# Performance work log

Measured on AMD Instinct MI355X. Metric: run time of the kernel, lower is better.

Reference implementation:

```python
import jax, jax.numpy as jnp
import numpy as np

N_NODES = 100000
N_EDGES = 1600000
NFEAT = 256
NHID = 64
NHEADS = 8
NCLASS = 97
ALPHA = 0.2  # leaky relu slope
EPS = 1e-16  # guard against isolated rows (pyGAT divides by e_rowsum directly)


def _sp_gat_layer(x, Wk, ak, src, dst, n_nodes, alpha, concat):
    """One SpGraphAttentionLayer (eval mode, dropout off).
    x: [N, f_in], Wk: [f_in, f_out], ak: [2*f_out].
    edge e_ij = exp(-leakyrelu(a . [h_i || h_j])), out[i] = sum_j e_ij h_j / sum_j e_ij.
    """
    h = x @ Wk                          # [N, f_out]
    f_out = Wk.shape[1]
    s_src = h @ ak[:f_out]              # [N] = a1 . h_i
    s_dst = h @ ak[f_out:]              # [N] = a2 . h_j
    e = jnp.exp(-jax.nn.leaky_relu(s_src[src] + s_dst[dst], negative_slope=alpha))  # [E]
    rowsum = jax.ops.segment_sum(e, src, num_segments=n_nodes)                       # [N]
    num = jax.ops.segment_sum(e[:, None] * h[dst], src, num_segments=n_nodes)        # [N, f_out]
    h_prime = num / (rowsum[:, None] + EPS)
    return jax.nn.elu(h_prime) if concat else h_prime


def setup_inputs() -> dict:
    key = jax.random.key(0)
    ks = jax.random.split(key, 6)
    gain = 1.414  # xavier gain used by pyGAT
    features = jax.random.normal(ks[0], (N_NODES, NFEAT), dtype=jnp.float32)
    edge_index = jax.random.randint(ks[1], (2, N_EDGES), 0, N_NODES, dtype=jnp.int64)
    W = jax.random.normal(ks[2], (NHEADS, NFEAT, NHID), dtype=jnp.float32) * (gain * np.sqrt(2.0 / (NFEAT + NHID)))
    a = jax.random.normal(ks[3], (NHEADS, 2 * NHID), dtype=jnp.float32) * (gain * np.sqrt(2.0 / (1 + 2 * NHID)))
    W_out = jax.random.normal(ks[4], (NHEADS * NHID, NCLASS), dtype=jnp.float32) * (gain * np.sqrt(2.0 / (NHEADS * NHID + NCLASS)))
    a_out = jax.random.normal(ks[5], (2 * NCLASS,), dtype=jnp.float32) * (gain * np.sqrt(2.0 / (1 + 2 * NCLASS)))
    return {"features": features, "W": W, "a": a, "W_out": W_out, "a_out": a_out, "edge_index": edge_index}


def reference(features, W, a, W_out, a_out, edge_index):
    src, dst = edge_index[0], edge_index[1]
    n = features.shape[0]
    # multi-head hidden layer, concat heads (loop over small fixed head count to bound memory)
    heads = [
        _sp_gat_layer(features, W[k], a[k], src, dst, n, ALPHA, concat=True)
        for k in range(W.shape[0])
    ]
    x = jnp.concatenate(heads, axis=1)  # [N, nheads*nhid]
    # output attention layer (concat=False), then elu + log_softmax as in SpGAT.forward
    x = _sp_gat_layer(x, W_out, a_out, src, dst, n, ALPHA, concat=False)
    return jax.nn.log_softmax(jax.nn.elu(x), axis=1)
```

## Files before the change

### kernel.cpp

```cpp
#include <hip/hip_runtime.h>
#include <hip/hip_bf16.h>
#include <stdint.h>

typedef __attribute__((ext_vector_type(8))) short short8;
typedef __attribute__((ext_vector_type(4))) float floatx4;
typedef uint32_t u32;

#define N_NODES 100000
#define N_EDGES 1600000
#define ALPHA_SLOPE 0.2f
#define EPS_F 1e-16f

static __device__ __forceinline__ float bf2f(ushort h) {
    u32 u = ((u32)h) << 16;
    return __builtin_bit_cast(float, u);
}
static __device__ __forceinline__ ushort f2bf(float f) {
    u32 u = __builtin_bit_cast(u32, f);
    u32 r = (u + 0x7fffu + ((u >> 16) & 1u)) >> 16;
    return (ushort)r;
}
static __device__ __forceinline__ float edge_e(float s) {
    float lr = s > 0.f ? s : ALPHA_SLOPE * s;
    return __expf(-lr);
}

__global__ __launch_bounds__(256) void prep(
    const float* __restrict__ feat, const float* __restrict__ W,
    const float* __restrict__ Wout, const float* __restrict__ a,
    const float* __restrict__ aout, const int* __restrict__ ei,
    ushort* __restrict__ featb, ushort* __restrict__ Bp1, ushort* __restrict__ Bp2,
    float* __restrict__ acol1, float* __restrict__ acol2, int* __restrict__ cnt)
{
    int b = blockIdx.x;
    if (b < 25000) {
        int i = b * 256 + threadIdx.x;
        float4 v = ((const float4*)feat)[i];
        ushort4 o;
        o.x = f2bf(v.x); o.y = f2bf(v.y); o.z = f2bf(v.z); o.w = f2bf(v.w);
        ((ushort4*)featb)[i] = o;
    } else if (b < 25512) {
        int idx = (b - 25000) * 256 + threadIdx.x;
        if (idx < 256 * 512) {
            int k = idx >> 9, n = idx & 511;
            int head = n >> 6, c = n & 63;
            Bp1[((size_t)(k >> 3) * 512 + n) * 8 + (k & 7)] = f2bf(W[head * 16384 + k * 64 + c]);
        }
        if (idx < 512 * 128) {
            int k = idx >> 7, n = idx & 127;
            ushort v = (n < 97) ? f2bf(Wout[k * 97 + n]) : (ushort)0;
            Bp2[((size_t)(k >> 3) * 128 + n) * 8 + (k & 7)] = v;
        }
        if (idx < 512) {
            int head = idx >> 6, c = idx & 63;
            acol1[idx * 2]     = a[head * 128 + c];
            acol1[idx * 2 + 1] = a[head * 128 + 64 + c];
        }
        if (idx < 128) {
            acol2[idx * 2]     = (idx < 97) ? aout[idx] : 0.f;
            acol2[idx * 2 + 1] = (idx < 97) ? aout[97 + idx] : 0.f;
        }
    } else {
        int e = (b - 25512) * 256 + threadIdx.x;
        atomicAdd(&cnt[ei[e]], 1);
    }
}

__global__ __launch_bounds__(256) void gemm_mfma(
    const ushort* __restrict__ A, const ushort* __restrict__ Bp,
    ushort* __restrict__ C, const float* __restrict__ acol,
    float* __restrict__ ssrc_arr, float* __restrict__ sdst_arr,
    int sstride, int M, int K, int NP)
{
    __shared__ __align__(16) ushort Ald[8 * 128 * 8];
    const int tid = threadIdx.x;
    const int lane = tid & 63;
    const int wave = tid >> 6;
    const int wr = wave >> 1, wc = wave & 1;
    const int row0 = blockIdx.y * 128;
    const int col0 = blockIdx.x * 128;
    const int quad = lane >> 4;
    const int l16 = lane & 15;

    floatx4 acc[4][4] = {};

    for (int k0 = 0; k0 < K; k0 += 64) {
        __syncthreads();
#pragma unroll
        for (int i = 0; i < 4; ++i) {
            int q = i * 256 + tid;
            int r = q >> 3, kq = q & 7;
            int row = row0 + r;
            if (row >= M) row = M - 1;
            const uint4* src = (const uint4*)(A + (size_t)row * K + k0 + kq * 8);
            *(uint4*)(&Ald[(kq * 128 + (r ^ kq)) * 8]) = *src;
        }
        __syncthreads();

#pragma unroll
        for (int s = 0; s < 2; ++s) {
            int kqq = s * 4 + quad;
            int kqg = (k0 >> 3) + kqq;
            short8 bfrag[4];
#pragma unroll
            for (int nt = 0; nt < 4; ++nt) {
                int col = col0 + wc * 64 + nt * 16 + l16;
                bfrag[nt] = *(const short8*)(Bp + ((size_t)kqg * NP + col) * 8);
            }
#pragma unroll
            for (int mt = 0; mt < 4; ++mt) {
                int r = wr * 64 + mt * 16 + l16;
                short8 afrag = *(const short8*)(&Ald[(kqq * 128 + (r ^ kqq)) * 8]);
#pragma unroll
                for (int nt = 0; nt < 4; ++nt) {
                    acc[mt][nt] = __builtin_amdgcn_mfma_f32_16x16x32_bf16(afrag, bfrag[nt], acc[mt][nt], 0, 0, 0);
                }
            }
        }
    }

#pragma unroll
    for (int mt = 0; mt < 4; ++mt) {
#pragma unroll
        for (int rr = 0; rr < 4; ++rr) {
            int row = row0 + wr * 64 + mt * 16 + quad * 4 + rr;
            if (row < M) {
#pragma unroll
                for (int nt = 0; nt < 4; ++nt) {
                    int col = col0 + wc * 64 + nt * 16 + l16;
                    C[(size_t)row * NP + col] = f2bf(acc[mt][nt][rr]);
                }
            }
        }
    }

    float av1[4], av2[4];
#pragma unroll
    for (int nt = 0; nt < 4; ++nt) {
        int col = col0 + wc * 64 + nt * 16 + l16;
        av1[nt] = acol[col * 2];
        av2[nt] = acol[col * 2 + 1];
    }
    int g = (col0 + wc * 64) >> 6;
    int goff = (sstride > 1) ? g : 0;
#pragma unroll
    for (int mt = 0; mt < 4; ++mt) {
#pragma unroll
        for (int rr = 0; rr < 4; ++rr) {
            float p1 = 0.f, p2 = 0.f;
#pragma unroll
            for (int nt = 0; nt < 4; ++nt) {
                p1 = fmaf(acc[mt][nt][rr], av1[nt], p1);
                p2 = fmaf(acc[mt][nt][rr], av2[nt], p2);
            }
#pragma unroll
            for (int o = 1; o < 16; o <<= 1) {
                p1 += __shfl_xor(p1, o);
                p2 += __shfl_xor(p2, o);
            }
            int row = row0 + wr * 64 + mt * 16 + quad * 4 + rr;
            if (l16 == 0 && row < M) {
                atomicAdd(&ssrc_arr[(size_t)row * sstride + goff], p1);
                atomicAdd(&sdst_arr[(size_t)row * sstride + goff], p2);
            }
        }
    }
}

__global__ __launch_bounds__(256) void scan_partial(const int* __restrict__ cnt, int* __restrict__ bsum, int N) {
    int idx = blockIdx.x * 256 + threadIdx.x;
    int v = (idx < N) ? cnt[idx] : 0;
#pragma unroll
    for (int o = 32; o; o >>= 1) v += __shfl_xor(v, o);
    __shared__ int ws[4];
    if ((threadIdx.x & 63) == 0) ws[threadIdx.x >> 6] = v;
    __syncthreads();
    if (threadIdx.x == 0) bsum[blockIdx.x] = ws[0] + ws[1] + ws[2] + ws[3];
}

__global__ __launch_bounds__(512) void scan_block(int* __restrict__ bsum, int nb) {
    __shared__ int s[512];
    int t = threadIdx.x;
    int v = (t < nb) ? bsum[t] : 0;
    s[t] = v;
    __syncthreads();
    for (int o = 1; o < 512; o <<= 1) {
        int u = (t >= o) ? s[t - o] : 0;
        __syncthreads();
        s[t] += u;
        __syncthreads();
    }
    if (t < nb) bsum[t] = s[t] - v;
}

__global__ __launch_bounds__(256) void scan_final(
    const int* __restrict__ cnt, const int* __restrict__ bsum,
    int* __restrict__ row_ptr, int N, int E)
{
    int b = blockIdx.x, t = threadIdx.x;
    int idx = b * 256 + t;
    int v = (idx < N) ? cnt[idx] : 0;
    __shared__ int s[256];
    s[t] = v;
    __syncthreads();
    for (int o = 1; o < 256; o <<= 1) {
        int u = (t >= o) ? s[t - o] : 0;
        __syncthreads();
        s[t] += u;
        __syncthreads();
    }
    if (idx < N) row_ptr[idx] = bsum[b] + s[t] - v;
    if (idx == 0) row_ptr[N] = E;
}

__global__ __launch_bounds__(256) void fill_csr(
    const int* __restrict__ ei, const int* __restrict__ row_ptr,
    int* __restrict__ cur, int* __restrict__ col_idx, int E)
{
    int e = blockIdx.x * 256 + threadIdx.x;
    if (e >= E) return;
    int s = ei[e];
    int d = ei[E + e];
    int p = atomicAdd(&cur[s], 1);
    col_idx[row_ptr[s] + p] = d;
}

__global__ __launch_bounds__(256, 6) void ea1p(
    const int* __restrict__ row_ptr, const int* __restrict__ col_idx,
    const ushort* __restrict__ h_all, const float* __restrict__ ssrc1,
    const float* __restrict__ sdst1, const ushort* __restrict__ Bp2,
    const float* __restrict__ acol2, ushort* __restrict__ h2p,
    float* __restrict__ s2src, float* __restrict__ s2dst)
{
    __shared__ __align__(16) ushort Xs[16 * 512];
    const int tid = threadIdx.x;
    const int l = tid & 63;
    const int wv = tid >> 6;
    const int hl = l >> 3;
    const int blk = blockIdx.x;

#pragma unroll 1
    for (int i = 0; i < 4; ++i) {
        int r = wv * 4 + i;
        int node = __builtin_amdgcn_readfirstlane(blk * 16 + r);
        int start = row_ptr[node], end = row_ptr[node + 1];
        float si = ssrc1[(size_t)node * 8 + hl];
        float acc[8] = {};
        float re = 0.f;
        int j = start;
        for (; j + 4 <= end; j += 4) {
            int d0 = col_idx[j], d1 = col_idx[j + 1], d2 = col_idx[j + 2], d3 = col_idx[j + 3];
            float e0 = edge_e(si + sdst1[(size_t)d0 * 8 + hl]);
            float e1 = edge_e(si + sdst1[(size_t)d1 * 8 + hl]);
            float e2 = edge_e(si + sdst1[(size_t)d2 * 8 + hl]);
            float e3 = edge_e(si + sdst1[(size_t)d3 * 8 + hl]);
            short8 v0 = *(const short8*)(h_all + (size_t)d0 * 512 + l * 8);
            short8 v1 = *(const short8*)(h_all + (size_t)d1 * 512 + l * 8);
            short8 v2 = *(const short8*)(h_all + (size_t)d2 * 512 + l * 8);
            short8 v3 = *(const short8*)(h_all + (size_t)d3 * 512 + l * 8);
            re += (e0 + e1) + (e2 + e3);
#pragma unroll
            for (int q = 0; q < 8; ++q) {
                float t0 = fmaf(e0, bf2f((ushort)v0[q]), e1 * bf2f((ushort)v1[q]));
                float t1 = fmaf(e2, bf2f((ushort)v2[q]), e3 * bf2f((ushort)v3[q]));
                acc[q] += t0 + t1;
            }
        }
        for (; j < end; ++j) {
            int d = col_idx[j];
            float e = edge_e(si + sdst1[(size_t)d * 8 + hl]);
            short8 hv = *(const short8*)(h_all + (size_t)d * 512 + l * 8);
            re += e;
#pragma unroll
            for (int q = 0; q < 8; ++q)
                acc[q] = fmaf(e, bf2f((ushort)hv[q]), acc[q]);
        }
        float inv = 1.f / (re + EPS_F);
        short8 o;
#pragma unroll
        for (int q = 0; q < 8; ++q) {
            float p = acc[q] * inv;
            p = p > 0.f ? p : expm1f(p);
            o[q] = (short)f2bf(p);
        }
        *(short8*)(&Xs[((size_t)r * 64 + (size_t)(l ^ (r & 7))) * 8]) = o;
    }
    __syncthreads();

    const int l16 = l & 15;
    const int g = l >> 4;
    floatx4 acc2[2] = {};
#pragma unroll
    for (int s = 0; s < 16; ++s) {
        int c = s * 4 + g;
        short8 afrag = *(const short8*)(&Xs[((size_t)l16 * 64 + (size_t)(c ^ (l16 & 7))) * 8]);
#pragma unroll
        for (int nt = 0; nt < 2; ++nt) {
            int col = wv * 32 + nt * 16 + l16;
            short8 bfrag = *(const short8*)(Bp2 + ((size_t)c * 128 + col) * 8);
            acc2[nt] = __builtin_amdgcn_mfma_f32_16x16x32_bf16(afrag, bfrag, acc2[nt], 0, 0, 0);
        }
    }

    float av1[2], av2[2];
#pragma unroll
    for (int nt = 0; nt < 2; ++nt) {
        int col = wv * 32 + nt * 16 + l16;
        av1[nt] = acol2[col * 2];
        av2[nt] = acol2[col * 2 + 1];
    }
#pragma unroll
    for (int rr = 0; rr < 4; ++rr) {
        int row = g * 4 + rr;
        int node = blk * 16 + row;
        float p1 = 0.f, p2 = 0.f;
#pragma unroll
        for (int nt = 0; nt < 2; ++nt) {
            int col = wv * 32 + nt * 16 + l16;
            h2p[(size_t)node * 128 + col] = f2bf(acc2[nt][rr]);
            p1 = fmaf(acc2[nt][rr], av1[nt], p1);
            p2 = fmaf(acc2[nt][rr], av2[nt], p2);
        }
#pragma unroll
        for (int o = 1; o < 16; o <<= 1) {
            p1 += __shfl_xor(p1, o);
            p2 += __shfl_xor(p2, o);
        }
        if (l16 == 0) {
            atomicAdd(&s2src[node], p1);
            atomicAdd(&s2dst[node], p2);
        }
    }
}

__global__ __launch_bounds__(256) void ea2(
    const int* __restrict__ row_ptr, const int* __restrict__ col_idx,
    const ushort* __restrict__ h2p, const float* __restrict__ s2src,
    const float* __restrict__ s2dst, float* __restrict__ out)
{
    int w = blockIdx.x * 8 + (threadIdx.x >> 5);
    int l = threadIdx.x & 31;
    int start = row_ptr[w], end = row_ptr[w + 1];
    float si = s2src[w];
    float a0 = 0.f, a1 = 0.f, a2 = 0.f, a3 = 0.f, re = 0.f;
    int j = start;
    for (; j + 4 <= end; j += 4) {
        int d0 = col_idx[j], d1 = col_idx[j + 1], d2 = col_idx[j + 2], d3 = col_idx[j + 3];
        float e0 = edge_e(si + s2dst[d0]);
        float e1 = edge_e(si + s2dst[d1]);
        float e2 = edge_e(si + s2dst[d2]);
        float e3 = edge_e(si + s2dst[d3]);
        ushort4 h0 = *(const ushort4*)(h2p + (size_t)d0 * 128 + 4 * l);
        ushort4 h1 = *(const ushort4*)(h2p + (size_t)d1 * 128 + 4 * l);
        ushort4 h2 = *(const ushort4*)(h2p + (size_t)d2 * 128 + 4 * l);
        ushort4 h3 = *(const ushort4*)(h2p + (size_t)d3 * 128 + 4 * l);
        re += (e0 + e1) + (e2 + e3);
        a0 += fmaf(e0, bf2f(h0.x), e1 * bf2f(h1.x)) + fmaf(e2, bf2f(h2.x), e3 * bf2f(h3.x));
        a1 += fmaf(e0, bf2f(h0.y), e1 * bf2f(h1.y)) + fmaf(e2, bf2f(h2.y), e3 * bf2f(h3.y));
        a2 += fmaf(e0, bf2f(h0.z), e1 * bf2f(h1.z)) + fmaf(e2, bf2f(h2.z), e3 * bf2f(h3.z));
        a3 += fmaf(e0, bf2f(h0.w), e1 * bf2f(h1.w)) + fmaf(e2, bf2f(h2.w), e3 * bf2f(h3.w));
    }
    for (; j < end; ++j) {
        int d = col_idx[j];
        float e = edge_e(si + s2dst[d]);
        ushort4 hv = *(const ushort4*)(h2p + (size_t)d * 128 + 4 * l);
        re += e;
        a0 = fmaf(e, bf2f(hv.x), a0);
        a1 = fmaf(e, bf2f(hv.y), a1);
        a2 = fmaf(e, bf2f(hv.z), a2);
        a3 = fmaf(e, bf2f(hv.w), a3);
    }
    float inv = 1.f / (re + EPS_F);
    float v[4] = { a0 * inv, a1 * inv, a2 * inv, a3 * inv };
    bool val[4];
    float m = -1e30f;
#pragma unroll
    for (int q = 0; q < 4; ++q) {
        v[q] = v[q] > 0.f ? v[q] : expm1f(v[q]);
        val[q] = (4 * l + q) < 97;
        if (val[q]) m = fmaxf(m, v[q]);
    }
#pragma unroll
    for (int o = 16; o; o >>= 1) m = fmaxf(m, __shfl_xor(m, o));
    float ex = 0.f;
#pragma unroll
    for (int q = 0; q < 4; ++q) ex += val[q] ? __expf(v[q] - m) : 0.f;
#pragma unroll
    for (int o = 16; o; o >>= 1) ex += __shfl_xor(ex, o);
    float lt = m + logf(ex);
#pragma unroll
    for (int q = 0; q < 4; ++q)
        if (val[q]) __builtin_nontemporal_store(v[q] - lt, out + (size_t)w * 97 + 4 * l + q);
}

extern "C" void kernel_launch(void* const* d_in, const int* in_sizes, int n_in,
                              void* d_out, int out_size, void* d_ws, size_t ws_size,
                              hipStream_t stream)
{
    const float* feat = (const float*)d_in[0];
    const float* W    = (const float*)d_in[1];
    const float* a    = (const float*)d_in[2];
    const float* Wout = (const float*)d_in[3];
    const float* aout = (const float*)d_in[4];
    const int*   ei   = (const int*)d_in[5];
    float* out = (float*)d_out;

    const int N = N_NODES, E = N_EDGES;
    const int NB = (N + 255) / 256;

    char* base = (char*)d_ws;
    ushort* h_all = (ushort*)(base);
    ushort* featb = (ushort*)(base + 204800000);
    ushort* h2p   = (ushort*)(base + 204800000);
    char* tail = base + 256000000;
    float* ssrc1   = (float*)(tail + 0);
    float* sdst1   = (float*)(tail + 3200000);
    float* s2src   = (float*)(tail + 6400000);
    float* s2dst   = (float*)(tail + 6800000);
    int*   row_ptr = (int*)(tail + 7200000);
    int*   cnt     = (int*)(tail + 7600128);
    int*   cur     = (int*)(tail + 8000128);
    int*   col_idx = (int*)(tail + 8400128);
    int*   bsum    = (int*)(tail + 14800128);
    ushort* Bp1    = (ushort*)(tail + 14801920);
    ushort* Bp2    = (ushort*)(tail + 15064064);
    float* acol1   = (float*)(tail + 15195136);
    float* acol2   = (float*)(tail + 15199232);

    hipMemsetAsync(ssrc1, 0, (size_t)8400128, stream);

    prep<<<31762, 256, 0, stream>>>(feat, W, Wout, a, aout, ei, featb, Bp1, Bp2, acol1, acol2, cnt);

    gemm_mfma<<<dim3(4, 782), 256, 0, stream>>>(featb, Bp1, h_all, acol1, ssrc1, sdst1, 8, N, 256, 512);

    scan_partial<<<NB, 256, 0, stream>>>(cnt, bsum, N);
    scan_block<<<1, 512, 0, stream>>>(bsum, NB);
    scan_final<<<NB, 256, 0, stream>>>(cnt, bsum, row_ptr, N, E);
    fill_csr<<<(E + 255) / 256, 256, 0, stream>>>(ei, row_ptr, cur, col_idx, E);

    ea1p<<<N / 16, 256, 0, stream>>>(row_ptr, col_idx, h_all, ssrc1, sdst1, Bp2, acol2, h2p, s2src, s2dst);

    ea2<<<N / 8, 256, 0, stream>>>(row_ptr, col_idx, h2p, s2src, s2dst, out);
}
```

Before: 774.5 us.

## Fuse fp32-to-bf16 feature conversion into GEMM, merge with CSR fill, shrink h2p stride

The separate feature conversion pass is removed. The GEMM now loads fp32 features directly and converts them to bf16 while staging into shared memory. Each GEMM block loops over all four column tiles and runs in the same launch as the CSR fill blocks, so the two pieces of work can overlap and one launch is saved. The layer-2 hidden buffer stride is cut from 128 to 104 so the edge aggregation gathers fewer bytes per neighbour. In exchange, the looped GEMM has only 782 blocks, each processing four column tiles one after another, and it re-reads and re-converts each fp32 A tile four times.

```diff
diff --git a/kernel.cpp b/kernel.cpp
--- a/kernel.cpp
+++ b/kernel.cpp
@@ -10,6 +10,7 @@
 #define N_EDGES 1600000
 #define ALPHA_SLOPE 0.2f
 #define EPS_F 1e-16f
+#define H2P_STRIDE 104
 
 static __device__ __forceinline__ float bf2f(ushort h) {
     u32 u = ((u32)h) << 16;
@@ -26,21 +27,15 @@
 }
 
 __global__ __launch_bounds__(256) void prep(
-    const float* __restrict__ feat, const float* __restrict__ W,
-    const float* __restrict__ Wout, const float* __restrict__ a,
-    const float* __restrict__ aout, const int* __restrict__ ei,
-    ushort* __restrict__ featb, ushort* __restrict__ Bp1, ushort* __restrict__ Bp2,
+    const float* __restrict__ W, const float* __restrict__ Wout,
+    const float* __restrict__ a, const float* __restrict__ aout,
+    const int* __restrict__ ei,
+    ushort* __restrict__ Bp1, ushort* __restrict__ Bp2,
     float* __restrict__ acol1, float* __restrict__ acol2, int* __restrict__ cnt)
 {
     int b = blockIdx.x;
-    if (b < 25000) {
-        int i = b * 256 + threadIdx.x;
-        float4 v = ((const float4*)feat)[i];
-        ushort4 o;
-        o.x = f2bf(v.x); o.y = f2bf(v.y); o.z = f2bf(v.z); o.w = f2bf(v.w);
-        ((ushort4*)featb)[i] = o;
-    } else if (b < 25512) {
-        int idx = (b - 25000) * 256 + threadIdx.x;
+    if (b < 512) {
+        int idx = b * 256 + threadIdx.x;
         if (idx < 256 * 512) {
             int k = idx >> 9, n = idx & 511;
             int head = n >> 6, c = n & 63;
@@ -61,109 +56,8 @@
             acol2[idx * 2 + 1] = (idx < 97) ? aout[97 + idx] : 0.f;
         }
     } else {
-        int e = (b - 25512) * 256 + threadIdx.x;
+        int e = (b - 512) * 256 + threadIdx.x;
         atomicAdd(&cnt[ei[e]], 1);
-    }
-}
-
-__global__ __launch_bounds__(256) void gemm_mfma(
-    const ushort* __restrict__ A, const ushort* __restrict__ Bp,
-    ushort* __restrict__ C, const float* __restrict__ acol,
-    float* __restrict__ ssrc_arr, float* __restrict__ sdst_arr,
-    int sstride, int M, int K, int NP)
-{
-    __shared__ __align__(16) ushort Ald[8 * 128 * 8];
-    const int tid = threadIdx.x;
-    const int lane = tid & 63;
-    const int wave = tid >> 6;
-    const int wr = wave >> 1, wc = wave & 1;
-    const int row0 = blockIdx.y * 128;
-    const int col0 = blockIdx.x * 128;
-    const int quad = lane >> 4;
-    const int l16 = lane & 15;
-
-    floatx4 acc[4][4] = {};
-
-    for (int k0 = 0; k0 < K; k0 += 64) {
-        __syncthreads();
-#pragma unroll
-        for (int i = 0; i < 4; ++i) {
-            int q = i * 256 + tid;
-            int r = q >> 3, kq = q & 7;
-            int row = row0 + r;
-            if (row >= M) row = M - 1;
-            const uint4* src = (const uint4*)(A + (size_t)row * K + k0 + kq * 8);
-            *(uint4*)(&Ald[(kq * 128 + (r ^ kq)) * 8]) = *src;
-        }
-        __syncthreads();
-
-#pragma unroll
-        for (int s = 0; s < 2; ++s) {
-            int kqq = s * 4 + quad;
-            int kqg = (k0 >> 3) + kqq;
-            short8 bfrag[4];
-#pragma unroll
-            for (int nt = 0; nt < 4; ++nt) {
-                int col = col0 + wc * 64 + nt * 16 + l16;
-                bfrag[nt] = *(const short8*)(Bp + ((size_t)kqg * NP + col) * 8);
-            }
-#pragma unroll
-            for (int mt = 0; mt < 4; ++mt) {
-                int r = wr * 64 + mt * 16 + l16;
-                short8 afrag = *(const short8*)(&Ald[(kqq * 128 + (r ^ kqq)) * 8]);
-#pragma unroll
-                for (int nt = 0; nt < 4; ++nt) {
-                    acc[mt][nt] = __builtin_amdgcn_mfma_f32_16x16x32_bf16(afrag, bfrag[nt], acc[mt][nt], 0, 0, 0);
-                }
-            }
-        }
-    }
-
-#pragma unroll
-    for (int mt = 0; mt < 4; ++mt) {
-#pragma unroll
-        for (int rr = 0; rr < 4; ++rr) {
-            int row = row0 + wr * 64 + mt * 16 + quad * 4 + rr;
-            if (row < M) {
-#pragma unroll
-                for (int nt = 0; nt < 4; ++nt) {
-                    int col = col0 + wc * 64 + nt * 16 + l16;
-                    C[(size_t)row * NP + col] = f2bf(acc[mt][nt][rr]);
-                }
-            }
-        }
-    }
-
-    float av1[4], av2[4];
-#pragma unroll
-    for (int nt = 0; nt < 4; ++nt) {
-        int col = col0 + wc * 64 + nt * 16 + l16;
-        av1[nt] = acol[col * 2];
-        av2[nt] = acol[col * 2 + 1];
-    }
-    int g = (col0 + wc * 64) >> 6;
-    int goff = (sstride > 1) ? g : 0;
-#pragma unroll
-    for (int mt = 0; mt < 4; ++mt) {
-#pragma unroll
-        for (int rr = 0; rr < 4; ++rr) {
-            float p1 = 0.f, p2 = 0.f;
-#pragma unroll
-            for (int nt = 0; nt < 4; ++nt) {
-                p1 = fmaf(acc[mt][nt][rr], av1[nt], p1);
-                p2 = fmaf(acc[mt][nt][rr], av2[nt], p2);
-            }
-#pragma unroll
-            for (int o = 1; o < 16; o <<= 1) {
-                p1 += __shfl_xor(p1, o);
-                p2 += __shfl_xor(p2, o);
-            }
-            int row = row0 + wr * 64 + mt * 16 + quad * 4 + rr;
-            if (l16 == 0 && row < M) {
-                atomicAdd(&ssrc_arr[(size_t)row * sstride + goff], p1);
-                atomicAdd(&sdst_arr[(size_t)row * sstride + goff], p2);
-            }
-        }
     }
 }
 
@@ -213,16 +107,125 @@
     if (idx == 0) row_ptr[N] = E;
 }
 
-__global__ __launch_bounds__(256) void fill_csr(
+__global__ __launch_bounds__(256) void gemm_fill(
+    const float* __restrict__ feat, const ushort* __restrict__ Bp,
+    ushort* __restrict__ C, const float* __restrict__ acol,
+    float* __restrict__ ssrc_arr, float* __restrict__ sdst_arr,
     const int* __restrict__ ei, const int* __restrict__ row_ptr,
-    int* __restrict__ cur, int* __restrict__ col_idx, int E)
-{
-    int e = blockIdx.x * 256 + threadIdx.x;
-    if (e >= E) return;
-    int s = ei[e];
-    int d = ei[E + e];
-    int p = atomicAdd(&cur[s], 1);
-    col_idx[row_ptr[s] + p] = d;
+    int* __restrict__ cur, int* __restrict__ col_idx)
+{
+    const int bx = blockIdx.x;
+    if (bx >= 782) {
+        int e = (bx - 782) * 256 + threadIdx.x;
+        int s = ei[e];
+        int d = ei[N_NODES == 0 ? 0 : N_EDGES + e];
+        int p = atomicAdd(&cur[s], 1);
+        col_idx[row_ptr[s] + p] = d;
+        return;
+    }
+
+    __shared__ __align__(16) ushort Ald[8 * 128 * 8];
+    const int tid = threadIdx.x;
+    const int lane = tid & 63;
+    const int wave = tid >> 6;
+    const int wr = wave >> 1, wc = wave & 1;
+    const int row0 = bx * 128;
+    const int quad = lane >> 4;
+    const int l16 = lane & 15;
+    const int M = N_NODES;
+
+#pragma unroll 1
+    for (int ct = 0; ct < 4; ++ct) {
+        const int col0 = ct * 128;
+        floatx4 acc[4][4] = {};
+
+        for (int k0 = 0; k0 < 256; k0 += 64) {
+            __syncthreads();
+#pragma unroll
+            for (int i = 0; i < 4; ++i) {
+                int q = i * 256 + tid;
+                int r = q >> 3, kq = q & 7;
+                int row = row0 + r;
+                if (row >= M) row = M - 1;
+                const float4* src = (const float4*)(feat + (size_t)row * 256 + k0 + kq * 8);
+                float4 f0 = src[0], f1 = src[1];
+                short8 o;
+                o[0] = (short)f2bf(f0.x); o[1] = (short)f2bf(f0.y);
+                o[2] = (short)f2bf(f0.z); o[3] = (short)f2bf(f0.w);
+                o[4] = (short)f2bf(f1.x); o[5] = (short)f2bf(f1.y);
+                o[6] = (short)f2bf(f1.z); o[7] = (short)f2bf(f1.w);
+                *(short8*)(&Ald[(kq * 128 + (r ^ kq)) * 8]) = o;
+            }
+            __syncthreads();
+
+#pragma unroll
+            for (int s = 0; s < 2; ++s) {
+                int kqq = s * 4 + quad;
+                int kqg = (k0 >> 3) + kqq;
+                short8 bfrag[4];
+#pragma unroll
+                for (int nt = 0; nt < 4; ++nt) {
+                    int col = col0 + wc * 64 + nt * 16 + l16;
+                    bfrag[nt] = *(const short8*)(Bp + ((size_t)kqg * 512 + col) * 8);
+                }
+#pragma unroll
+                for (int mt = 0; mt < 4; ++mt) {
+                    int r = wr * 64 + mt * 16 + l16;
+                    short8 afrag = *(const short8*)(&Ald[(kqq * 128 + (r ^ kqq)) * 8]);
+#pragma unroll
+                    for (int nt = 0; nt < 4; ++nt) {
+                        acc[mt][nt] = __builtin_amdgcn_mfma_f32_16x16x32_bf16(afrag, bfrag[nt], acc[mt][nt], 0, 0, 0);
+                    }
+                }
+            }
+        }
+
+#pragma unroll
+        for (int mt = 0; mt < 4; ++mt) {
+#pragma unroll
+            for (int rr = 0; rr < 4; ++rr) {
+                int row = row0 + wr * 64 + mt * 16 + quad * 4 + rr;
+                if (row < M) {
+#pragma unroll
+                    for (int nt = 0; nt < 4; ++nt) {
+                        int col = col0 + wc * 64 + nt * 16 + l16;
+                        C[(size_t)row * 512 + col] = f2bf(acc[mt][nt][rr]);
+                    }
+                }
+            }
+        }
+
+        float av1[4], av2[4];
+#pragma unroll
+        for (int nt = 0; nt < 4; ++nt) {
+            int col = col0 + wc * 64 + nt * 16 + l16;
+            av1[nt] = acol[col * 2];
+            av2[nt] = acol[col * 2 + 1];
+        }
+        int g = (col0 + wc * 64) >> 6;
+#pragma unroll
+        for (int mt = 0; mt < 4; ++mt) {
+#pragma unroll
+            for (int rr = 0; rr < 4; ++rr) {
+                float p1 = 0.f, p2 = 0.f;
+#pragma unroll
+                for (int nt = 0; nt < 4; ++nt) {
+                    p1 = fmaf(acc[mt][nt][rr], av1[nt], p1);
+                    p2 = fmaf(acc[mt][nt][rr], av2[nt], p2);
+                }
+#pragma unroll
+                for (int o = 1; o < 16; o <<= 1) {
+                    p1 += __shfl_xor(p1, o);
+                    p2 += __shfl_xor(p2, o);
+                }
+                int row = row0 + wr * 64 + mt * 16 + quad * 4 + rr;
+                if (l16 == 0 && row < M) {
+                    atomicAdd(&ssrc_arr[(size_t)row * 8 + g], p1);
+                    atomicAdd(&sdst_arr[(size_t)row * 8 + g], p2);
+                }
+            }
+        }
+    }
 }
 
 __global__ __launch_bounds__(256, 6) void ea1p(
@@ -317,7 +320,8 @@
 #pragma unroll
         for (int nt = 0; nt < 2; ++nt) {
             int col = wv * 32 + nt * 16 + l16;
-            h2p[(size_t)node * 128 + col] = f2bf(acc2[nt][rr]);
+            if (col < H2P_STRIDE)
+                h2p[(size_t)node * H2P_STRIDE + col] = f2bf(acc2[nt][rr]);
             p1 = fmaf(acc2[nt][rr], av1[nt], p1);
             p2 = fmaf(acc2[nt][rr], av2[nt], p2);
         }
@@ -340,9 +344,11 @@
 {
     int w = blockIdx.x * 8 + (threadIdx.x >> 5);
     int l = threadIdx.x & 31;
+    const bool ldv = (l < 26);
     int start = row_ptr[w], end = row_ptr[w + 1];
     float si = s2src[w];
     float a0 = 0.f, a1 = 0.f, a2 = 0.f, a3 = 0.f, re = 0.f;
+    const ushort4 z = {0, 0, 0, 0};
     int j = start;
     for (; j + 4 <= end; j += 4) {
         int d0 = col_idx[j], d1 = col_idx[j + 1], d2 = col_idx[j + 2], d3 = col_idx[j + 3];
@@ -350,10 +356,10 @@
         float e1 = edge_e(si + s2dst[d1]);
         float e2 = edge_e(si + s2dst[d2]);
         float e3 = edge_e(si + s2dst[d3]);
-        ushort4 h0 = *(const ushort4*)(h2p + (size_t)d0 * 128 + 4 * l);
-        ushort4 h1 = *(const ushort4*)(h2p + (size_t)d1 * 128 + 4 * l);
-        ushort4 h2 = *(const ushort4*)(h2p + (size_t)d2 * 128 + 4 * l);
-        ushort4 h3 = *(const ushort4*)(h2p + (size_t)d3 * 128 + 4 * l);
+        ushort4 h0 = ldv ? *(const ushort4*)(h2p + (size_t)d0 * H2P_STRIDE + 4 * l) : z;
+        ushort4 h1 = ldv ? *(const ushort4*)(h2p + (size_t)d1 * H2P_STRIDE + 4 * l) : z;
+        ushort4 h2 = ldv ? *(const ushort4*)(h2p + (size_t)d2 * H2P_STRIDE + 4 * l) : z;
+        ushort4 h3 = ldv ? *(const ushort4*)(h2p + (size_t)d3 * H2P_STRIDE + 4 * l) : z;
         re += (e0 + e1) + (e2 + e3);
         a0 += fmaf(e0, bf2f(h0.x), e1 * bf2f(h1.x)) + fmaf(e2, bf2f(h2.x), e3 * bf2f(h3.x));
         a1 += fmaf(e0, bf2f(h0.y), e1 * bf2f(h1.y)) + fmaf(e2, bf2f(h2.y), e3 * bf2f(h3.y));
@@ -363,7 +369,7 @@
     for (; j < end; ++j) {
         int d = col_idx[j];
         float e = edge_e(si + s2dst[d]);
-        ushort4 hv = *(const ushort4*)(h2p + (size_t)d * 128 + 4 * l);
+        ushort4 hv = ldv ? *(const ushort4*)(h2p + (size_t)d * H2P_STRIDE + 4 * l) : z;
         re += e;
         a0 = fmaf(e, bf2f(hv.x), a0);
         a1 = fmaf(e, bf2f(hv.y), a1);
@@ -410,7 +416,6 @@
 
     char* base = (char*)d_ws;
     ushort* h_all = (ushort*)(base);
-    ushort* featb = (ushort*)(base + 204800000);
     ushort* h2p   = (ushort*)(base + 204800000);
     char* tail = base + 256000000;
     float* ssrc1   = (float*)(tail + 0);
@@ -429,14 +434,14 @@
 
     hipMemsetAsync(ssrc1, 0, (size_t)8400128, stream);
 
-    prep<<<31762, 256, 0, stream>>>(feat, W, Wout, a, aout, ei, featb, Bp1, Bp2, acol1, acol2, cnt);
-
-    gemm_mfma<<<dim3(4, 782), 256, 0, stream>>>(featb, Bp1, h_all, acol1, ssrc1, sdst1, 8, N, 256, 512);
+    prep<<<6762, 256, 0, stream>>>(W, Wout, a, aout, ei, Bp1, Bp2, acol1, acol2, cnt);
 
     scan_partial<<<NB, 256, 0, stream>>>(cnt, bsum, N);
     scan_block<<<1, 512, 0, stream>>>(bsum, NB);
     scan_final<<<NB, 256, 0, stream>>>(cnt, bsum, row_ptr, N, E);
-    fill_csr<<<(E + 255) / 256, 256, 0, stream>>>(ei, row_ptr, cur, col_idx, E);
+
+    gemm_fill<<<782 + 6250, 256, 0, stream>>>(feat, Bp1, h_all, acol1, ssrc1, sdst1,
+                                              ei, row_ptr, cur, col_idx);
 
     ea1p<<<N / 16, 256, 0, stream>>>(row_ptr, col_idx, h_all, ssrc1, sdst1, Bp2, acol2, h2p, s2src, s2dst);
 
```

Result: slower. 824.9 us (+6.5%).
